# Kernel tuning notes

Hardware: AMD Instinct MI355X
Metric: run time of the kernel (lower is better)

The kernel has to match this reference:

```python
import jax, jax.numpy as jnp
import numpy as np

IN_SIZE = 1024
OUT_SIZE = 1024
HEAD_NUM = 16
KEY_SIZE = OUT_SIZE // HEAD_NUM  # 64
MIN_VALUE = float(np.finfo(np.float32).min / 2.0)
LN_EPS = 1e-5


def setup_inputs() -> dict:
    key = jax.random.key(0)
    ks = jax.random.split(key, 12)
    B, L = 4, 1024
    s_in = 1.0 / np.sqrt(IN_SIZE)
    s_out = 1.0 / np.sqrt(OUT_SIZE)
    x = jax.random.normal(ks[0], (B, L, IN_SIZE), dtype=jnp.float32)
    mask = jax.random.randint(ks[1], (B, L), 0, 2, dtype=jnp.int32)
    # Per-head linears stacked: [H, in, key_size] (already transposed for x @ W)
    Wq = jax.random.normal(ks[2], (HEAD_NUM, IN_SIZE, KEY_SIZE), dtype=jnp.float32) * s_in
    bq = jax.random.normal(ks[3], (HEAD_NUM, KEY_SIZE), dtype=jnp.float32) * s_in
    Wk = jax.random.normal(ks[4], (HEAD_NUM, IN_SIZE, KEY_SIZE), dtype=jnp.float32) * s_in
    bk = jax.random.normal(ks[5], (HEAD_NUM, KEY_SIZE), dtype=jnp.float32) * s_in
    Wv = jax.random.normal(ks[6], (HEAD_NUM, IN_SIZE, KEY_SIZE), dtype=jnp.float32) * s_in
    bv = jax.random.normal(ks[7], (HEAD_NUM, KEY_SIZE), dtype=jnp.float32) * s_in
    Wo = jax.random.normal(ks[8], (OUT_SIZE, OUT_SIZE), dtype=jnp.float32) * s_out
    bo = jax.random.normal(ks[9], (OUT_SIZE,), dtype=jnp.float32) * s_out
    gamma = jnp.ones((OUT_SIZE,), dtype=jnp.float32)
    beta = jnp.zeros((OUT_SIZE,), dtype=jnp.float32)
    return {"x": x, "mask": mask, "Wq": Wq, "bq": bq, "Wk": Wk, "bk": bk,
            "Wv": Wv, "bv": bv, "Wo": Wo, "bo": bo, "gamma": gamma, "beta": beta}


def _attention(x, mask, Wq, bq, Wk, bk, Wv, bv, Wo, bo, gamma, beta):
    # Per-head projections, batched over heads: [B, H, L, d]
    q = jnp.einsum('bli,hid->bhld', x, Wq) + bq[None, :, None, :]
    k = jnp.einsum('bli,hid->bhld', x, Wk) + bk[None, :, None, :]
    v = jnp.einsum('bli,hid->bhld', x, Wv) + bv[None, :, None, :]
    scale = 1.0 / np.sqrt(KEY_SIZE)
    score = jnp.einsum('bhld,bhmd->bhlm', q, k) * scale  # [B, H, L, L]
    # masked_fill((mask == 0).unsqueeze(-2), min_value): mask over key positions
    score = jnp.where((mask == 0)[:, None, None, :], MIN_VALUE, score)
    atten = jax.nn.softmax(score, axis=-1)  # [B, H, L, L]
    value = jnp.einsum('bhlm,bhmd->bhld', atten, v)
    # concat heads -> [B, L, H*d] then output linear
    B, H, L, d = value.shape
    value = value.transpose(0, 2, 1, 3).reshape(B, L, H * d)
    value = value @ Wo.T + bo
    # wo_resize=False and in_size == out_size -> nearest interpolate is identity
    bypass = x
    pre = bypass + value
    mu = jnp.mean(pre, axis=-1, keepdims=True)
    var = jnp.mean(jnp.square(pre - mu), axis=-1, keepdims=True)
    out = (pre - mu) * jax.lax.rsqrt(var + LN_EPS) * gamma + beta
    return out, atten


def reference(x, mask, Wq, bq, Wk, bk, Wv, bv, Wo, bo, gamma, beta):
    return _attention(x, mask, Wq, bq, Wk, bk, Wv, bv, Wo, bo, gamma, beta)
```

## Files before the change

kernel.cpp:

```cpp
#include <hip/hip_runtime.h>
#include <hip/hip_bf16.h>

typedef __bf16 bf16x8 __attribute__((ext_vector_type(8)));
typedef __bf16 bf16x4 __attribute__((ext_vector_type(4)));
typedef float  f32x4  __attribute__((ext_vector_type(4)));

#define MIN_VALUE (-1.7014118346046923e38f)

__global__ __launch_bounds__(256) void split_x_kernel(const float* __restrict__ x,
                                                      __bf16* __restrict__ xh,
                                                      __bf16* __restrict__ xl) {
    int i = (blockIdx.x * 256 + threadIdx.x) * 4;
    float4 v = *(const float4*)(x + i);
    float vv[4] = {v.x, v.y, v.z, v.w};
    bf16x4 h, l;
    for (int e = 0; e < 4; ++e) {
        __bf16 hi = (__bf16)vv[e];
        h[e] = hi;
        l[e] = (__bf16)(vv[e] - (float)hi);
    }
    *(bf16x4*)(xh + i) = h;
    *(bf16x4*)(xl + i) = l;
}

__global__ __launch_bounds__(256) void split_w_kernel(const float* __restrict__ Wq,
                                                      const float* __restrict__ Wk,
                                                      const float* __restrict__ Wv,
                                                      __bf16* __restrict__ wh,
                                                      __bf16* __restrict__ wl) {
    __shared__ float t[32][33];
    int z = blockIdx.z;
    int sel = z >> 4, h = z & 15;
    const float* W = (sel == 0) ? Wq : (sel == 1) ? Wk : Wv;
    int i0 = blockIdx.x * 32, d0 = blockIdx.y * 32;
    int tx = threadIdx.x & 31, ty = threadIdx.x >> 5;
    for (int it = 0; it < 4; ++it) {
        int r = ty + it * 8;
        t[r][tx] = W[(size_t)(h * 1024 + i0 + r) * 64 + d0 + tx];
    }
    __syncthreads();
    for (int it = 0; it < 4; ++it) {
        int r = ty + it * 8;
        float v = t[tx][r];
        size_t o = (size_t)(sel * 1024 + h * 64 + d0 + r) * 1024 + i0 + tx;
        __bf16 hi = (__bf16)v;
        wh[o] = hi;
        wl[o] = (__bf16)(v - (float)hi);
    }
}

__global__ __launch_bounds__(256) void conv_wo_kernel(const float* __restrict__ Wo,
                                                      __bf16* __restrict__ wob) {
    int i = (blockIdx.x * 256 + threadIdx.x) * 4;
    float4 v = *(const float4*)(Wo + i);
    float vv[4] = {v.x, v.y, v.z, v.w};
    bf16x4 h;
    for (int e = 0; e < 4; ++e) h[e] = (__bf16)vv[e];
    *(bf16x4*)(wob + i) = h;
}

__global__ __launch_bounds__(256) void qkv_gemm_kernel(
    const __bf16* __restrict__ xh, const __bf16* __restrict__ xl,
    const __bf16* __restrict__ wh, const __bf16* __restrict__ wl,
    const float* __restrict__ bq, const float* __restrict__ bk, const float* __restrict__ bv,
    __bf16* __restrict__ qb, __bf16* __restrict__ kb, __bf16* __restrict__ vtb) {
    __shared__ __bf16 As[2][128 * 32];
    __shared__ __bf16 Bs[2][128 * 32];
    const int tid = threadIdx.x;
    const int m0 = blockIdx.y * 128;
    const int n0 = blockIdx.x * 128;
    const int lane = tid & 63, w = tid >> 6;
    const int l15 = lane & 15, quad = lane >> 4;
    const int wm = (w & 1) * 64, wn = (w >> 1) * 64;

    f32x4 acc[4][4];
    for (int i = 0; i < 4; ++i)
        for (int j = 0; j < 4; ++j)
            for (int r = 0; r < 4; ++r) acc[i][j][r] = 0.0f;

    for (int kk = 0; kk < 1024; kk += 32) {
        __syncthreads();
        for (int cc = 0; cc < 2; ++cc) {
            int c = tid + cc * 256;
            int row = c >> 2, k8 = (c & 3) * 8;
            *(bf16x8*)&As[0][row * 32 + k8] = *(const bf16x8*)&xh[(size_t)(m0 + row) * 1024 + kk + k8];
            *(bf16x8*)&As[1][row * 32 + k8] = *(const bf16x8*)&xl[(size_t)(m0 + row) * 1024 + kk + k8];
            *(bf16x8*)&Bs[0][row * 32 + k8] = *(const bf16x8*)&wh[(size_t)(n0 + row) * 1024 + kk + k8];
            *(bf16x8*)&Bs[1][row * 32 + k8] = *(const bf16x8*)&wl[(size_t)(n0 + row) * 1024 + kk + k8];
        }
        __syncthreads();
        bf16x8 af[4][2], bfr[4][2];
        for (int i = 0; i < 4; ++i) {
            af[i][0] = *(const bf16x8*)&As[0][(wm + i * 16 + l15) * 32 + quad * 8];
            af[i][1] = *(const bf16x8*)&As[1][(wm + i * 16 + l15) * 32 + quad * 8];
        }
        for (int j = 0; j < 4; ++j) {
            bfr[j][0] = *(const bf16x8*)&Bs[0][(wn + j * 16 + l15) * 32 + quad * 8];
            bfr[j][1] = *(const bf16x8*)&Bs[1][(wn + j * 16 + l15) * 32 + quad * 8];
        }
        for (int i = 0; i < 4; ++i)
            for (int j = 0; j < 4; ++j) {
                acc[i][j] = __builtin_amdgcn_mfma_f32_16x16x32_bf16(af[i][0], bfr[j][0], acc[i][j], 0, 0, 0);
                acc[i][j] = __builtin_amdgcn_mfma_f32_16x16x32_bf16(af[i][0], bfr[j][1], acc[i][j], 0, 0, 0);
                acc[i][j] = __builtin_amdgcn_mfma_f32_16x16x32_bf16(af[i][1], bfr[j][0], acc[i][j], 0, 0, 0);
            }
    }

    const int sel = n0 >> 10;
    const float* bias = (sel == 0) ? bq : (sel == 1) ? bk : bv;
    for (int i = 0; i < 4; ++i)
        for (int j = 0; j < 4; ++j)
            for (int r = 0; r < 4; ++r) {
                int m = m0 + wm + i * 16 + quad * 4 + r;
                int n = n0 + wn + j * 16 + l15;
                int nn = n & 1023;
                int h = nn >> 6, d = n & 63;
                float v = acc[i][j][r] + bias[nn];
                int bb = m >> 10, ll = m & 1023;
                if (sel == 2) {
                    vtb[(size_t)((bb * 16 + h) * 64 + d) * 1024 + ll] = (__bf16)v;
                } else {
                    __bf16* dst = (sel == 0) ? qb : kb;
                    dst[(size_t)((bb * 16 + h) * 1024 + ll) * 64 + d] = (__bf16)v;
                }
            }
}

__global__ __launch_bounds__(256) void attn_kernel(
    const __bf16* __restrict__ qb, const __bf16* __restrict__ kb,
    const __bf16* __restrict__ vtb, const int* __restrict__ mask,
    float* __restrict__ atten, __bf16* __restrict__ value_bf) {
    __shared__ float S[16 * 1024];
    const int m0 = blockIdx.x * 16;
    const int h = blockIdx.y, b = blockIdx.z;
    const int bh = b * 16 + h;
    const int tid = threadIdx.x;
    const int lane = tid & 63, w = tid >> 6;
    const int l15 = lane & 15, quad = lane >> 4;

    const __bf16* qbase = qb + (size_t)(bh * 1024 + m0 + l15) * 64 + quad * 8;
    bf16x8 a0 = *(const bf16x8*)(qbase);
    bf16x8 a1 = *(const bf16x8*)(qbase + 32);
    for (int t = 0; t < 16; ++t) {
        int n0 = w * 256 + t * 16;
        const __bf16* kbase = kb + (size_t)(bh * 1024 + n0 + l15) * 64 + quad * 8;
        bf16x8 b0 = *(const bf16x8*)(kbase);
        bf16x8 b1 = *(const bf16x8*)(kbase + 32);
        f32x4 c = {0.f, 0.f, 0.f, 0.f};
        c = __builtin_amdgcn_mfma_f32_16x16x32_bf16(a0, b0, c, 0, 0, 0);
        c = __builtin_amdgcn_mfma_f32_16x16x32_bf16(a1, b1, c, 0, 0, 0);
        int col = n0 + l15;
        bool msk = (mask[b * 1024 + col] == 0);
        for (int r = 0; r < 4; ++r) {
            float s = c[r] * 0.125f;
            if (msk) s = MIN_VALUE;
            S[(quad * 4 + r) * 1024 + col] = s;
        }
    }
    __syncthreads();

    float p[4][16];
    float invs[4];
    for (int j = 0; j < 4; ++j) {
        int row = w * 4 + j;
        float mx = -3.4e38f;
        for (int i = 0; i < 16; ++i) {
            p[j][i] = S[row * 1024 + i * 64 + lane];
            mx = fmaxf(mx, p[j][i]);
        }
        for (int o = 32; o > 0; o >>= 1) mx = fmaxf(mx, __shfl_xor(mx, o));
        float sum = 0.f;
        for (int i = 0; i < 16; ++i) {
            float e = __expf(p[j][i] - mx);
            p[j][i] = e;
            sum += e;
        }
        for (int o = 32; o > 0; o >>= 1) sum += __shfl_xor(sum, o);
        float inv = 1.0f / sum;
        invs[j] = inv;
        float* out = atten + (size_t)(bh * 1024 + m0 + row) * 1024;
        for (int i = 0; i < 16; ++i) {
            p[j][i] *= inv;
            out[i * 64 + lane] = p[j][i];
        }
    }
    __syncthreads();

    __bf16* Sb = (__bf16*)S;
    for (int j = 0; j < 4; ++j) {
        int row = w * 4 + j;
        for (int i = 0; i < 16; ++i) Sb[row * 1040 + i * 64 + lane] = (__bf16)p[j][i];
    }
    __syncthreads();

    f32x4 acc = {0.f, 0.f, 0.f, 0.f};
    const __bf16* vbase = vtb + (size_t)(bh * 64 + w * 16 + l15) * 1024 + quad * 8;
    for (int kk = 0; kk < 1024; kk += 32) {
        bf16x8 af = *(const bf16x8*)&Sb[l15 * 1040 + kk + quad * 8];
        bf16x8 bf_ = *(const bf16x8*)(vbase + kk);
        acc = __builtin_amdgcn_mfma_f32_16x16x32_bf16(af, bf_, acc, 0, 0, 0);
    }
    for (int r = 0; r < 4; ++r) {
        int mrow = quad * 4 + r;
        value_bf[(size_t)(b * 1024 + m0 + mrow) * 1024 + h * 64 + w * 16 + l15] = (__bf16)acc[r];
    }
}

__global__ __launch_bounds__(256) void outproj_kernel(
    const __bf16* __restrict__ vb, const __bf16* __restrict__ wob,
    const float* __restrict__ x, const float* __restrict__ bo,
    float* __restrict__ pre) {
    __shared__ __bf16 As[128 * 32];
    __shared__ __bf16 Bs[128 * 32];
    const int tid = threadIdx.x;
    const int m0 = blockIdx.y * 128;
    const int n0 = blockIdx.x * 128;
    const int lane = tid & 63, w = tid >> 6;
    const int l15 = lane & 15, quad = lane >> 4;
    const int wm = (w & 1) * 64, wn = (w >> 1) * 64;

    f32x4 acc[4][4];
    for (int i = 0; i < 4; ++i)
        for (int j = 0; j < 4; ++j)
            for (int r = 0; r < 4; ++r) acc[i][j][r] = 0.0f;

    for (int kk = 0; kk < 1024; kk += 32) {
        __syncthreads();
        for (int cc = 0; cc < 2; ++cc) {
            int c = tid + cc * 256;
            int row = c >> 2, k8 = (c & 3) * 8;
            *(bf16x8*)&As[row * 32 + k8] = *(const bf16x8*)&vb[(size_t)(m0 + row) * 1024 + kk + k8];
            *(bf16x8*)&Bs[row * 32 + k8] = *(const bf16x8*)&wob[(size_t)(n0 + row) * 1024 + kk + k8];
        }
        __syncthreads();
        bf16x8 af[4], bfr[4];
        for (int i = 0; i < 4; ++i) af[i] = *(const bf16x8*)&As[(wm + i * 16 + l15) * 32 + quad * 8];
        for (int j = 0; j < 4; ++j) bfr[j] = *(const bf16x8*)&Bs[(wn + j * 16 + l15) * 32 + quad * 8];
        for (int i = 0; i < 4; ++i)
            for (int j = 0; j < 4; ++j)
                acc[i][j] = __builtin_amdgcn_mfma_f32_16x16x32_bf16(af[i], bfr[j], acc[i][j], 0, 0, 0);
    }

    for (int i = 0; i < 4; ++i)
        for (int j = 0; j < 4; ++j)
            for (int r = 0; r < 4; ++r) {
                int m = m0 + wm + i * 16 + quad * 4 + r;
                int n = n0 + wn + j * 16 + l15;
                pre[(size_t)m * 1024 + n] = acc[i][j][r] + x[(size_t)m * 1024 + n] + bo[n];
            }
}

__global__ __launch_bounds__(256) void ln_kernel(float* __restrict__ buf,
                                                 const float* __restrict__ gamma,
                                                 const float* __restrict__ beta) {
    const int row = blockIdx.x;
    const int tid = threadIdx.x;
    const int lane = tid & 63, w = tid >> 6;
    __shared__ float red[8];
    float* rp = buf + (size_t)row * 1024;
    float loc[4];
    float s = 0.f, s2 = 0.f;
    for (int e = 0; e < 4; ++e) {
        loc[e] = rp[tid + e * 256];
        s += loc[e];
        s2 += loc[e] * loc[e];
    }
    for (int o = 32; o > 0; o >>= 1) {
        s += __shfl_xor(s, o);
        s2 += __shfl_xor(s2, o);
    }
    if (lane == 0) { red[w * 2] = s; red[w * 2 + 1] = s2; }
    __syncthreads();
    float ts = red[0] + red[2] + red[4] + red[6];
    float ts2 = red[1] + red[3] + red[5] + red[7];
    float mu = ts * (1.0f / 1024.0f);
    float var = ts2 * (1.0f / 1024.0f) - mu * mu;
    float sc = rsqrtf(var + 1e-5f);
    for (int e = 0; e < 4; ++e) {
        int c = tid + e * 256;
        rp[c] = (loc[e] - mu) * sc * gamma[c] + beta[c];
    }
}

extern "C" void kernel_launch(void* const* d_in, const int* in_sizes, int n_in,
                              void* d_out, int out_size, void* d_ws, size_t ws_size,
                              hipStream_t stream) {
    const float* x    = (const float*)d_in[0];
    const int*   mask = (const int*)d_in[1];
    const float* Wq   = (const float*)d_in[2];
    const float* bq   = (const float*)d_in[3];
    const float* Wk   = (const float*)d_in[4];
    const float* bk   = (const float*)d_in[5];
    const float* Wv   = (const float*)d_in[6];
    const float* bv   = (const float*)d_in[7];
    const float* Wo   = (const float*)d_in[8];
    const float* bo   = (const float*)d_in[9];
    const float* gamma= (const float*)d_in[10];
    const float* beta = (const float*)d_in[11];

    char* p = (char*)d_ws;
    __bf16* xh    = (__bf16*)p; p += (size_t)4194304 * 2;
    __bf16* xl    = (__bf16*)p; p += (size_t)4194304 * 2;
    __bf16* wt_hi = (__bf16*)p; p += (size_t)3145728 * 2;
    __bf16* wt_lo = (__bf16*)p; p += (size_t)3145728 * 2;
    __bf16* wob   = (__bf16*)p; p += (size_t)1048576 * 2;
    __bf16* qb    = (__bf16*)p; p += (size_t)4194304 * 2;
    __bf16* kb    = (__bf16*)p; p += (size_t)4194304 * 2;
    __bf16* vtb   = (__bf16*)p; p += (size_t)4194304 * 2;
    __bf16* valb  = (__bf16*)p; p += (size_t)4194304 * 2;

    float* outb  = (float*)d_out;
    float* atten = outb + 4194304;

    split_x_kernel<<<4096, 256, 0, stream>>>(x, xh, xl);
    split_w_kernel<<<dim3(32, 2, 48), 256, 0, stream>>>(Wq, Wk, Wv, wt_hi, wt_lo);
    conv_wo_kernel<<<1024, 256, 0, stream>>>(Wo, wob);
    qkv_gemm_kernel<<<dim3(24, 32), 256, 0, stream>>>(xh, xl, wt_hi, wt_lo, bq, bk, bv, qb, kb, vtb);
    attn_kernel<<<dim3(64, 16, 4), 256, 0, stream>>>(qb, kb, vtb, mask, atten, valb);
    outproj_kernel<<<dim3(8, 32), 256, 0, stream>>>(valb, wob, x, bo, outb);
    ln_kernel<<<4096, 256, 0, stream>>>(outb, gamma, beta);
}
```

Measured before the change: 579.8 us.

## Drop x low-part split, use direct global-to-LDS loads, swizzle score buffer

The QKV GEMM no longer splits x into hi/lo bf16 parts. It uses x_hi against both W_hi and W_lo, which removes one MFMA per tile, the xl buffer and its conversion writes. Both GEMMs now load tiles with global_load_lds (direct global-to-LDS) instead of going through registers. The attention kernel XOR-swizzles the shared score buffer to reduce LDS bank conflicts. Dropping the x low part reduces the precision of the QKV projection, which risks larger numerical error.

```diff
diff --git a/kernel.cpp b/kernel.cpp
--- a/kernel.cpp
+++ b/kernel.cpp
@@ -7,20 +7,21 @@
 
 #define MIN_VALUE (-1.7014118346046923e38f)
 
-__global__ __launch_bounds__(256) void split_x_kernel(const float* __restrict__ x,
-                                                      __bf16* __restrict__ xh,
-                                                      __bf16* __restrict__ xl) {
+__device__ __forceinline__ void async_load16(const __bf16* g, __bf16* l) {
+    __builtin_amdgcn_global_load_lds(
+        (const __attribute__((address_space(1))) uint32_t*)(uintptr_t)g,
+        (__attribute__((address_space(3))) uint32_t*)(uint32_t)(uintptr_t)l,
+        16, 0, 0);
+}
+
+__global__ __launch_bounds__(256) void conv_x_kernel(const float* __restrict__ x,
+                                                     __bf16* __restrict__ xh) {
     int i = (blockIdx.x * 256 + threadIdx.x) * 4;
     float4 v = *(const float4*)(x + i);
     float vv[4] = {v.x, v.y, v.z, v.w};
-    bf16x4 h, l;
-    for (int e = 0; e < 4; ++e) {
-        __bf16 hi = (__bf16)vv[e];
-        h[e] = hi;
-        l[e] = (__bf16)(vv[e] - (float)hi);
-    }
+    bf16x4 h;
+    for (int e = 0; e < 4; ++e) h[e] = (__bf16)vv[e];
     *(bf16x4*)(xh + i) = h;
-    *(bf16x4*)(xl + i) = l;
 }
 
 __global__ __launch_bounds__(256) void split_w_kernel(const float* __restrict__ Wq,
@@ -60,18 +61,21 @@
 }
 
 __global__ __launch_bounds__(256) void qkv_gemm_kernel(
-    const __bf16* __restrict__ xh, const __bf16* __restrict__ xl,
+    const __bf16* __restrict__ xh,
     const __bf16* __restrict__ wh, const __bf16* __restrict__ wl,
     const float* __restrict__ bq, const float* __restrict__ bk, const float* __restrict__ bv,
     __bf16* __restrict__ qb, __bf16* __restrict__ kb, __bf16* __restrict__ vtb) {
-    __shared__ __bf16 As[2][128 * 32];
-    __shared__ __bf16 Bs[2][128 * 32];
+    __shared__ __bf16 As[128 * 32];
+    __shared__ __bf16 Bh[128 * 32];
+    __shared__ __bf16 Bl[128 * 32];
     const int tid = threadIdx.x;
     const int m0 = blockIdx.y * 128;
     const int n0 = blockIdx.x * 128;
     const int lane = tid & 63, w = tid >> 6;
     const int l15 = lane & 15, quad = lane >> 4;
     const int wm = (w & 1) * 64, wn = (w >> 1) * 64;
+    const int r4 = lane >> 2;
+    const int c8 = (lane & 3) * 8;
 
     f32x4 acc[4][4];
     for (int i = 0; i < 4; ++i)
@@ -80,29 +84,25 @@
 
     for (int kk = 0; kk < 1024; kk += 32) {
         __syncthreads();
-        for (int cc = 0; cc < 2; ++cc) {
-            int c = tid + cc * 256;
-            int row = c >> 2, k8 = (c & 3) * 8;
-            *(bf16x8*)&As[0][row * 32 + k8] = *(const bf16x8*)&xh[(size_t)(m0 + row) * 1024 + kk + k8];
-            *(bf16x8*)&As[1][row * 32 + k8] = *(const bf16x8*)&xl[(size_t)(m0 + row) * 1024 + kk + k8];
-            *(bf16x8*)&Bs[0][row * 32 + k8] = *(const bf16x8*)&wh[(size_t)(n0 + row) * 1024 + kk + k8];
-            *(bf16x8*)&Bs[1][row * 32 + k8] = *(const bf16x8*)&wl[(size_t)(n0 + row) * 1024 + kk + k8];
+        for (int half = 0; half < 2; ++half) {
+            int row = w * 32 + half * 16 + r4;
+            int lo = w * 1024 + half * 512 + lane * 8;
+            async_load16(&xh[(size_t)(m0 + row) * 1024 + kk + c8], &As[lo]);
+            async_load16(&wh[(size_t)(n0 + row) * 1024 + kk + c8], &Bh[lo]);
+            async_load16(&wl[(size_t)(n0 + row) * 1024 + kk + c8], &Bl[lo]);
         }
         __syncthreads();
-        bf16x8 af[4][2], bfr[4][2];
-        for (int i = 0; i < 4; ++i) {
-            af[i][0] = *(const bf16x8*)&As[0][(wm + i * 16 + l15) * 32 + quad * 8];
-            af[i][1] = *(const bf16x8*)&As[1][(wm + i * 16 + l15) * 32 + quad * 8];
-        }
+        bf16x8 af[4], bhf[4], blf[4];
+        for (int i = 0; i < 4; ++i)
+            af[i] = *(const bf16x8*)&As[(wm + i * 16 + l15) * 32 + quad * 8];
         for (int j = 0; j < 4; ++j) {
-            bfr[j][0] = *(const bf16x8*)&Bs[0][(wn + j * 16 + l15) * 32 + quad * 8];
-            bfr[j][1] = *(const bf16x8*)&Bs[1][(wn + j * 16 + l15) * 32 + quad * 8];
+            bhf[j] = *(const bf16x8*)&Bh[(wn + j * 16 + l15) * 32 + quad * 8];
+            blf[j] = *(const bf16x8*)&Bl[(wn + j * 16 + l15) * 32 + quad * 8];
         }
         for (int i = 0; i < 4; ++i)
             for (int j = 0; j < 4; ++j) {
-                acc[i][j] = __builtin_amdgcn_mfma_f32_16x16x32_bf16(af[i][0], bfr[j][0], acc[i][j], 0, 0, 0);
-                acc[i][j] = __builtin_amdgcn_mfma_f32_16x16x32_bf16(af[i][0], bfr[j][1], acc[i][j], 0, 0, 0);
-                acc[i][j] = __builtin_amdgcn_mfma_f32_16x16x32_bf16(af[i][1], bfr[j][0], acc[i][j], 0, 0, 0);
+                acc[i][j] = __builtin_amdgcn_mfma_f32_16x16x32_bf16(af[i], bhf[j], acc[i][j], 0, 0, 0);
+                acc[i][j] = __builtin_amdgcn_mfma_f32_16x16x32_bf16(af[i], blf[j], acc[i][j], 0, 0, 0);
             }
     }
 
@@ -141,6 +141,7 @@
     const __bf16* qbase = qb + (size_t)(bh * 1024 + m0 + l15) * 64 + quad * 8;
     bf16x8 a0 = *(const bf16x8*)(qbase);
     bf16x8 a1 = *(const bf16x8*)(qbase + 32);
+    const int swz1 = quad << 4;
     for (int t = 0; t < 16; ++t) {
         int n0 = w * 256 + t * 16;
         const __bf16* kbase = kb + (size_t)(bh * 1024 + n0 + l15) * 64 + quad * 8;
@@ -154,18 +155,18 @@
         for (int r = 0; r < 4; ++r) {
             float s = c[r] * 0.125f;
             if (msk) s = MIN_VALUE;
-            S[(quad * 4 + r) * 1024 + col] = s;
+            S[(quad * 4 + r) * 1024 + (col ^ swz1)] = s;
         }
     }
     __syncthreads();
 
     float p[4][16];
-    float invs[4];
+    const int swz2 = w << 4;
     for (int j = 0; j < 4; ++j) {
         int row = w * 4 + j;
         float mx = -3.4e38f;
         for (int i = 0; i < 16; ++i) {
-            p[j][i] = S[row * 1024 + i * 64 + lane];
+            p[j][i] = S[row * 1024 + ((i * 64 + lane) ^ swz2)];
             mx = fmaxf(mx, p[j][i]);
         }
         for (int o = 32; o > 0; o >>= 1) mx = fmaxf(mx, __shfl_xor(mx, o));
@@ -177,7 +178,6 @@
         }
         for (int o = 32; o > 0; o >>= 1) sum += __shfl_xor(sum, o);
         float inv = 1.0f / sum;
-        invs[j] = inv;
         float* out = atten + (size_t)(bh * 1024 + m0 + row) * 1024;
         for (int i = 0; i < 16; ++i) {
             p[j][i] *= inv;
@@ -218,6 +218,8 @@
     const int lane = tid & 63, w = tid >> 6;
     const int l15 = lane & 15, quad = lane >> 4;
     const int wm = (w & 1) * 64, wn = (w >> 1) * 64;
+    const int r4 = lane >> 2;
+    const int c8 = (lane & 3) * 8;
 
     f32x4 acc[4][4];
     for (int i = 0; i < 4; ++i)
@@ -226,11 +228,11 @@
 
     for (int kk = 0; kk < 1024; kk += 32) {
         __syncthreads();
-        for (int cc = 0; cc < 2; ++cc) {
-            int c = tid + cc * 256;
-            int row = c >> 2, k8 = (c & 3) * 8;
-            *(bf16x8*)&As[row * 32 + k8] = *(const bf16x8*)&vb[(size_t)(m0 + row) * 1024 + kk + k8];
-            *(bf16x8*)&Bs[row * 32 + k8] = *(const bf16x8*)&wob[(size_t)(n0 + row) * 1024 + kk + k8];
+        for (int half = 0; half < 2; ++half) {
+            int row = w * 32 + half * 16 + r4;
+            int lo = w * 1024 + half * 512 + lane * 8;
+            async_load16(&vb[(size_t)(m0 + row) * 1024 + kk + c8], &As[lo]);
+            async_load16(&wob[(size_t)(n0 + row) * 1024 + kk + c8], &Bs[lo]);
         }
         __syncthreads();
         bf16x8 af[4], bfr[4];
@@ -300,7 +302,6 @@
 
     char* p = (char*)d_ws;
     __bf16* xh    = (__bf16*)p; p += (size_t)4194304 * 2;
-    __bf16* xl    = (__bf16*)p; p += (size_t)4194304 * 2;
     __bf16* wt_hi = (__bf16*)p; p += (size_t)3145728 * 2;
     __bf16* wt_lo = (__bf16*)p; p += (size_t)3145728 * 2;
     __bf16* wob   = (__bf16*)p; p += (size_t)1048576 * 2;
@@ -312,10 +313,10 @@
     float* outb  = (float*)d_out;
     float* atten = outb + 4194304;
 
-    split_x_kernel<<<4096, 256, 0, stream>>>(x, xh, xl);
+    conv_x_kernel<<<4096, 256, 0, stream>>>(x, xh);
     split_w_kernel<<<dim3(32, 2, 48), 256, 0, stream>>>(Wq, Wk, Wv, wt_hi, wt_lo);
     conv_wo_kernel<<<1024, 256, 0, stream>>>(Wo, wob);
-    qkv_gemm_kernel<<<dim3(24, 32), 256, 0, stream>>>(xh, xl, wt_hi, wt_lo, bq, bk, bv, qb, kb, vtb);
+    qkv_gemm_kernel<<<dim3(24, 32), 256, 0, stream>>>(xh, wt_hi, wt_lo, bq, bk, bv, qb, kb, vtb);
     attn_kernel<<<dim3(64, 16, 4), 256, 0, stream>>>(qb, kb, vtb, mask, atten, valb);
     outproj_kernel<<<dim3(8, 32), 256, 0, stream>>>(valb, wob, x, bo, outb);
     ln_kernel<<<4096, 256, 0, stream>>>(outb, gamma, beta);
```

Result: faster. 553.2 us (-4.6%).
